# Kernel tuning notes

Measured on AMD Instinct MI355X. Metric: run time of the kernel, lower is better.

Reference implementation:

```python
import jax, jax.numpy as jnp
import numpy as np

B, T, D = 4, 2048, 1024
E, F, K = 8, 4096, 2  # num experts, ffn hidden, top-k


def setup_inputs() -> dict:
    key = jax.random.key(0)
    ks = jax.random.split(key, 7)
    s_in = 1.0 / np.sqrt(D)
    s_ff = 1.0 / np.sqrt(F)
    return {
        "x": jax.random.normal(ks[0], (B, T, D), dtype=jnp.float32),
        "Wg": jax.random.normal(ks[1], (D, E), dtype=jnp.float32) * s_in,
        "bg": jnp.zeros((E,), dtype=jnp.float32),
        "W1": jax.random.normal(ks[2], (E, D, F), dtype=jnp.float32) * s_in,
        "b1": jnp.zeros((E, F), dtype=jnp.float32),
        "W2": jax.random.normal(ks[3], (E, F, D), dtype=jnp.float32) * s_ff,
        "b2": jnp.zeros((E, D), dtype=jnp.float32),
    }


def reference(x, Wg, bg, W1, b1, W2, b2):
    # Gate: per-token expert logits [B, T, E]
    logits = jnp.einsum("btd,de->bte", x, Wg) + bg
    # Top-k per token, softmax over only the selected logits (as in the source)
    topv, topi = jax.lax.top_k(logits, K)          # [B, T, K]
    probs = jax.nn.softmax(topv, axis=-1)           # [B, T, K]
    out = jnp.zeros_like(x)
    # Loop over the small fixed expert set; each expert runs a dense MLP over
    # all tokens, masked/weighted by its routing probability (0 if unselected).
    for e in range(E):
        w = jnp.sum(probs * (topi == e), axis=-1)   # [B, T] combine weight
        h = jax.nn.gelu(jnp.einsum("btd,df->btf", x, W1[e]) + b1[e], approximate=False)
        y = jnp.einsum("btf,fd->btd", h, W2[e]) + b2[e]
        out = out + w[..., None] * y
    return out
```

## Files before the change

### kernel.cpp

```cpp
#include <hip/hip_runtime.h>
#include <cstdint>

#define B_ 4
#define T_ 2048
#define D_ 1024
#define E_ 8
#define F_ 4096
#define K_ 2
#define N_ (B_*T_)
#define NR_ (N_*K_)

#define TM 128
#define BK 64
#define MAXP (NR_ + E_*TM)
#define MAXMB (NR_/TM + E_)
#define MBPX (MAXMB/8)

typedef __attribute__((ext_vector_type(8))) short short8;
typedef __attribute__((ext_vector_type(4))) float f32x4;

typedef const __attribute__((address_space(1))) unsigned int* gp1_t;
typedef __attribute__((address_space(3))) unsigned int* lp3_t;

__device__ __forceinline__ void gl_lds16(const void* g, void* l) {
    __builtin_amdgcn_global_load_lds((gp1_t)g, (lp3_t)l, 16, 0, 0);
}

__device__ __forceinline__ unsigned short f2b(float f) {
    union { float f; unsigned int u; } v; v.f = f;
    unsigned int u = v.u;
    return (unsigned short)((u + 0x7FFFu + ((u >> 16) & 1u)) >> 16);
}

__device__ __forceinline__ float b2f(unsigned short u) {
    union { unsigned int i; float f; } v; v.i = ((unsigned int)u) << 16;
    return v.f;
}

__device__ __forceinline__ float gelu_exact(float x) {
    return 0.5f * x * (1.0f + erff(x * 0.70710678118654752440f));
}

__global__ __launch_bounds__(256) void gate_kernel(
    const float* __restrict__ x, const float* __restrict__ Wg,
    const float* __restrict__ bg, int* __restrict__ topi,
    float* __restrict__ topw, int* __restrict__ counts) {
    int tid  = threadIdx.x;
    int lane = tid & 63;
    int tok  = blockIdx.x * 4 + (tid >> 6);
    int e = lane & 7;
    int c = lane >> 3;
    const float4* xp = (const float4*)(x + (size_t)tok * D_ + c * 128);
    const float*  wp = Wg + (size_t)(c * 128) * E_ + e;
    float acc = 0.f;
    #pragma unroll 8
    for (int i = 0; i < 32; ++i) {
        float4 xv = xp[i];
        acc += xv.x * wp[(i*4+0)*E_];
        acc += xv.y * wp[(i*4+1)*E_];
        acc += xv.z * wp[(i*4+2)*E_];
        acc += xv.w * wp[(i*4+3)*E_];
    }
    acc += __shfl_xor(acc, 8, 64);
    acc += __shfl_xor(acc, 16, 64);
    acc += __shfl_xor(acc, 32, 64);
    float logit = acc + bg[e];
    float v1 = -3.4e38f, v2 = -3.4e38f; int i1 = -1, i2 = -1;
    for (int ee = 0; ee < 8; ++ee) {
        float le = __shfl(logit, ee, 64);
        if (le > v1) { v2 = v1; i2 = i1; v1 = le; i1 = ee; }
        else if (le > v2) { v2 = le; i2 = ee; }
    }
    if (lane == 0) {
        float p2 = expf(v2 - v1);
        float s  = 1.0f + p2;
        topi[tok*2]   = i1; topw[tok*2]   = 1.0f / s;
        topi[tok*2+1] = i2; topw[tok*2+1] = p2 / s;
        atomicAdd(&counts[i1], 1);
        atomicAdd(&counts[i2], 1);
    }
}

__global__ void scan_kernel(const int* __restrict__ counts,
                            int* __restrict__ offs, int* __restrict__ cursors,
                            int* __restrict__ mb_e, int* __restrict__ mb_m0) {
    if (threadIdx.x == 0) {
        int s = 0, mb = 0;
        for (int e = 0; e < E_; ++e) {
            offs[e] = s; cursors[e] = s;
            int nb = (counts[e] + TM - 1) / TM;
            for (int i = 0; i < nb; ++i) { mb_e[mb] = e; mb_m0[mb] = s + i*TM; ++mb; }
            s += nb * TM;
        }
        offs[E_] = s;
        for (int b = mb; b < MAXMB; ++b) mb_e[b] = -1;
    }
}

__global__ __launch_bounds__(256) void scatter_kernel(
    const int* __restrict__ topi, int* __restrict__ cursors,
    int* __restrict__ perm, int* __restrict__ slots) {
    int t = blockIdx.x * blockDim.x + threadIdx.x;
    int lane = threadIdx.x & 63;
    unsigned long long lanebit_m1 = (lane == 63) ? ~0ULL >> 1
                                  : ((1ULL << (lane & 63)) - 1ULL);
    lanebit_m1 = (1ULL << lane) - 1ULL;
    #pragma unroll
    for (int k = 0; k < K_; ++k) {
        int e = (t < N_) ? topi[t*2 + k] : -1;
        int pos = 0;
        #pragma unroll
        for (int ee = 0; ee < E_; ++ee) {
            unsigned long long mask = __ballot(e == ee);
            if (mask) {
                int leader = __ffsll((long long)mask) - 1;
                int base = 0;
                if (lane == leader)
                    base = atomicAdd(&cursors[ee], __popcll(mask));
                base = __shfl(base, leader, 64);
                if (e == ee)
                    pos = base + __popcll(mask & lanebit_m1);
            }
        }
        if (t < N_) {
            perm[pos] = t;
            slots[t*2 + k] = pos;
        }
    }
}

__global__ __launch_bounds__(256) void castx_kernel(
    const float* __restrict__ x, unsigned short* __restrict__ xb) {
    int i = blockIdx.x * blockDim.x + threadIdx.x;
    float4 v = ((const float4*)x)[i];
    ushort4 o; o.x = f2b(v.x); o.y = f2b(v.y); o.z = f2b(v.z); o.w = f2b(v.w);
    ((ushort4*)xb)[i] = o;
}

__global__ __launch_bounds__(256) void tcast_kernel(
    const float* __restrict__ src, unsigned short* __restrict__ dst, int R, int C) {
    __shared__ float tile[64][65];
    int rb = blockIdx.x * 64, cb = blockIdx.y * 64;
    const float* s = src + (size_t)blockIdx.z * R * C;
    unsigned short* d = dst + (size_t)blockIdx.z * R * C;
    int tx = threadIdx.x & 15, ty = threadIdx.x >> 4;
    #pragma unroll
    for (int i = 0; i < 4; ++i) {
        int r = ty + i*16;
        float4 v = *(const float4*)&s[(size_t)(rb + r) * C + cb + tx*4];
        tile[r][tx*4+0] = v.x; tile[r][tx*4+1] = v.y;
        tile[r][tx*4+2] = v.z; tile[r][tx*4+3] = v.w;
    }
    __syncthreads();
    #pragma unroll
    for (int i = 0; i < 4; ++i) {
        int c = ty + i*16;
        ushort4 o;
        o.x = f2b(tile[tx*4+0][c]);
        o.y = f2b(tile[tx*4+1][c]);
        o.z = f2b(tile[tx*4+2][c]);
        o.w = f2b(tile[tx*4+3][c]);
        *(ushort4*)&d[(size_t)(cb + c) * R + rb + tx*4] = o;
    }
}

__global__ __launch_bounds__(256, 4) void ffn1_kernel(
    const unsigned short* __restrict__ Xb, const unsigned short* __restrict__ W1t,
    const float* __restrict__ b1, const int* __restrict__ perm,
    const int* __restrict__ mb_e, const int* __restrict__ mb_m0,
    unsigned short* __restrict__ H) {
    int o   = blockIdx.x + gridDim.x * blockIdx.y;
    int xcd = o & 7;
    int j   = o >> 3;
    int mbi = xcd * MBPX + (j % MBPX);
    int nbi = j / MBPX;
    int e = mb_e[mbi];
    if (e < 0) return;
    int m0 = mb_m0[mbi];
    int n0 = nbi * 128;
    const unsigned short* Bw = W1t + (size_t)e * F_ * D_;

    __shared__ __align__(16) unsigned short lA[128*BK];
    __shared__ __align__(16) unsigned short lB[128*BK];

    int t = threadIdx.x;
    int lane = t & 63;
    int wv = t >> 6;
    int wrow = (wv >> 1) * 64, wcol = (wv & 1) * 64;
    int lr = lane & 15, q = lane >> 4;
    int xork = lr & 7;

    int sr = t >> 3;
    int sc = ((t & 7) ^ (sr & 7)) * 8;
    const unsigned short* pa[4];
    const unsigned short* pb[4];
    #pragma unroll
    for (int i = 0; i < 4; ++i) {
        int tok = perm[m0 + sr + 32*i];
        pa[i] = Xb + (size_t)tok * D_ + sc;
        pb[i] = Bw + (size_t)(n0 + sr + 32*i) * D_ + sc;
    }

    f32x4 acc[4][4];
    #pragma unroll
    for (int mi = 0; mi < 4; ++mi)
        #pragma unroll
        for (int ni = 0; ni < 4; ++ni)
            acc[mi][ni] = (f32x4){0.f, 0.f, 0.f, 0.f};

    for (int kk = 0; kk < D_/BK; ++kk) {
        int k0 = kk * BK;
        #pragma unroll
        for (int i = 0; i < 4; ++i) {
            gl_lds16(pa[i] + k0, &lA[i*2048 + t*8]);
            gl_lds16(pb[i] + k0, &lB[i*2048 + t*8]);
        }
        asm volatile("s_waitcnt vmcnt(0)" ::: "memory");
        __syncthreads();
        #pragma unroll
        for (int s = 0; s < 2; ++s) {
            short8 af[4], bf[4];
            #pragma unroll
            for (int mi = 0; mi < 4; ++mi)
                af[mi] = *(const short8*)&lA[(wrow + mi*16 + lr)*BK + (((s*4+q) ^ xork) * 8)];
            #pragma unroll
            for (int ni = 0; ni < 4; ++ni)
                bf[ni] = *(const short8*)&lB[(wcol + ni*16 + lr)*BK + (((s*4+q) ^ xork) * 8)];
            #pragma unroll
            for (int mi = 0; mi < 4; ++mi)
                #pragma unroll
                for (int ni = 0; ni < 4; ++ni)
                    acc[mi][ni] = __builtin_amdgcn_mfma_f32_16x16x32_bf16(
                        af[mi], bf[ni], acc[mi][ni], 0, 0, 0);
        }
        __syncthreads();
    }

    const float* b1e = b1 + (size_t)e * F_;
    #pragma unroll
    for (int mi = 0; mi < 4; ++mi) {
        int gr = m0 + wrow + mi*16 + q*4;
        #pragma unroll
        for (int ni = 0; ni < 4; ++ni) {
            int f = n0 + wcol + ni*16 + lr;
            float bb = b1e[f];
            #pragma unroll
            for (int r = 0; r < 4; ++r) {
                float h = gelu_exact(acc[mi][ni][r] + bb);
                H[(size_t)(gr + r) * F_ + f] = f2b(h);
            }
        }
    }
}

__global__ __launch_bounds__(256, 4) void ffn2_kernel(
    const unsigned short* __restrict__ H, const unsigned short* __restrict__ W2t,
    const float* __restrict__ b2,
    const int* __restrict__ mb_e, const int* __restrict__ mb_m0,
    unsigned short* __restrict__ Y) {
    int o   = blockIdx.x + gridDim.x * blockIdx.y;
    int xcd = o & 7;
    int j   = o >> 3;
    int mbi = xcd * MBPX + (j % MBPX);
    int nbi = j / MBPX;
    int e = mb_e[mbi];
    if (e < 0) return;
    int m0 = mb_m0[mbi];
    int n0 = nbi * 128;
    const unsigned short* Bw = W2t + (size_t)e * D_ * F_;

    __shared__ __align__(16) unsigned short lA[128*BK];
    __shared__ __align__(16) unsigned short lB[128*BK];

    int t = threadIdx.x;
    int lane = t & 63;
    int wv = t >> 6;
    int wrow = (wv >> 1) * 64, wcol = (wv & 1) * 64;
    int lr = lane & 15, q = lane >> 4;
    int xork = lr & 7;

    int sr = t >> 3;
    int sc = ((t & 7) ^ (sr & 7)) * 8;
    const unsigned short* pa[4];
    const unsigned short* pb[4];
    #pragma unroll
    for (int i = 0; i < 4; ++i) {
        pa[i] = H  + (size_t)(m0 + sr + 32*i) * F_ + sc;
        pb[i] = Bw + (size_t)(n0 + sr + 32*i) * F_ + sc;
    }

    f32x4 acc[4][4];
    #pragma unroll
    for (int mi = 0; mi < 4; ++mi)
        #pragma unroll
        for (int ni = 0; ni < 4; ++ni)
            acc[mi][ni] = (f32x4){0.f, 0.f, 0.f, 0.f};

    for (int kk = 0; kk < F_/BK; ++kk) {
        int k0 = kk * BK;
        #pragma unroll
        for (int i = 0; i < 4; ++i) {
            gl_lds16(pa[i] + k0, &lA[i*2048 + t*8]);
            gl_lds16(pb[i] + k0, &lB[i*2048 + t*8]);
        }
        asm volatile("s_waitcnt vmcnt(0)" ::: "memory");
        __syncthreads();
        #pragma unroll
        for (int s = 0; s < 2; ++s) {
            short8 af[4], bf[4];
            #pragma unroll
            for (int mi = 0; mi < 4; ++mi)
                af[mi] = *(const short8*)&lA[(wrow + mi*16 + lr)*BK + (((s*4+q) ^ xork) * 8)];
            #pragma unroll
            for (int ni = 0; ni < 4; ++ni)
                bf[ni] = *(const short8*)&lB[(wcol + ni*16 + lr)*BK + (((s*4+q) ^ xork) * 8)];
            #pragma unroll
            for (int mi = 0; mi < 4; ++mi)
                #pragma unroll
                for (int ni = 0; ni < 4; ++ni)
                    acc[mi][ni] = __builtin_amdgcn_mfma_f32_16x16x32_bf16(
                        af[mi], bf[ni], acc[mi][ni], 0, 0, 0);
        }
        __syncthreads();
    }

    const float* b2e = b2 + (size_t)e * D_;
    #pragma unroll
    for (int mi = 0; mi < 4; ++mi) {
        int gr = m0 + wrow + mi*16 + q*4;
        #pragma unroll
        for (int ni = 0; ni < 4; ++ni) {
            int dcol = n0 + wcol + ni*16 + lr;
            float bb = b2e[dcol];
            #pragma unroll
            for (int r = 0; r < 4; ++r)
                Y[(size_t)(gr + r) * D_ + dcol] = f2b(acc[mi][ni][r] + bb);
        }
    }
}

__global__ __launch_bounds__(256) void combine_kernel(
    const unsigned short* __restrict__ Y, const int* __restrict__ slots,
    const float* __restrict__ topw, float* __restrict__ out) {
    int t  = blockIdx.x;
    int d4 = threadIdx.x * 4;
    int s0 = slots[t*2], s1 = slots[t*2+1];
    float w0 = topw[t*2], w1 = topw[t*2+1];
    ushort4 y0 = *(const ushort4*)&Y[(size_t)s0 * D_ + d4];
    ushort4 y1 = *(const ushort4*)&Y[(size_t)s1 * D_ + d4];
    float4 o;
    o.x = w0*b2f(y0.x) + w1*b2f(y1.x);
    o.y = w0*b2f(y0.y) + w1*b2f(y1.y);
    o.z = w0*b2f(y0.z) + w1*b2f(y1.z);
    o.w = w0*b2f(y0.w) + w1*b2f(y1.w);
    *(float4*)&out[(size_t)t * D_ + d4] = o;
}

extern "C" void kernel_launch(void* const* d_in, const int* in_sizes, int n_in,
                              void* d_out, int out_size, void* d_ws, size_t ws_size,
                              hipStream_t stream) {
    const float* x  = (const float*)d_in[0];
    const float* Wg = (const float*)d_in[1];
    const float* bg = (const float*)d_in[2];
    const float* W1 = (const float*)d_in[3];
    const float* b1 = (const float*)d_in[4];
    const float* W2 = (const float*)d_in[5];
    const float* b2 = (const float*)d_in[6];
    float* out = (float*)d_out;

    char* wsp = (char*)d_ws;
    size_t off = 0;
    auto alloc = [&](size_t bytes) {
        void* p = wsp + off;
        off += (bytes + 255) & ~(size_t)255;
        return p;
    };
    int*   topi    = (int*)  alloc((size_t)NR_*4);
    float* topw    = (float*)alloc((size_t)NR_*4);
    int*   slots   = (int*)  alloc((size_t)NR_*4);
    int*   counts  = (int*)  alloc(E_*4);
    int*   offs    = (int*)  alloc((E_+1)*4);
    int*   cursors = (int*)  alloc(E_*4);
    int*   mb_e    = (int*)  alloc(MAXMB*4);
    int*   mb_m0   = (int*)  alloc(MAXMB*4);
    int*   perm    = (int*)  alloc((size_t)MAXP*4);
    unsigned short* Xb  = (unsigned short*)alloc((size_t)N_*D_*2);
    unsigned short* W1t = (unsigned short*)alloc((size_t)E_*D_*F_*2);
    unsigned short* W2t = (unsigned short*)alloc((size_t)E_*D_*F_*2);
    unsigned short* Hb  = (unsigned short*)alloc((size_t)MAXP*F_*2);
    unsigned short* Yb  = (unsigned short*)alloc((size_t)MAXP*D_*2);

    hipMemsetAsync(counts, 0, E_*4, stream);
    hipMemsetAsync(perm, 0, (size_t)MAXP*4, stream);

    gate_kernel<<<N_/4, 256, 0, stream>>>(x, Wg, bg, topi, topw, counts);
    scan_kernel<<<1, 64, 0, stream>>>(counts, offs, cursors, mb_e, mb_m0);
    scatter_kernel<<<N_/256, 256, 0, stream>>>(topi, cursors, perm, slots);
    castx_kernel<<<(N_*(size_t)D_/4)/256, 256, 0, stream>>>(x, Xb);
    tcast_kernel<<<dim3(D_/64, F_/64, E_), 256, 0, stream>>>(W1, W1t, D_, F_);
    tcast_kernel<<<dim3(F_/64, D_/64, E_), 256, 0, stream>>>(W2, W2t, F_, D_);
    ffn1_kernel<<<dim3(MAXMB, F_/128), 256, 0, stream>>>(Xb, W1t, b1, perm, mb_e, mb_m0, Hb);
    ffn2_kernel<<<dim3(MAXMB, D_/128), 256, 0, stream>>>(Hb, W2t, b2, mb_e, mb_m0, Yb);
    combine_kernel<<<N_, 256, 0, stream>>>(Yb, slots, topw, out);
}
```

Before: 946.9 us.

## Double-buffer LDS tiles in expert GEMMs and fuse x cast into gate

Both expert FFN GEMM kernels now use two LDS buffers, prefetching the next K tile with global_load_lds while computing the current one. A partial vmcnt wait and raw s_barrier replace the full drain each iteration. Launch bounds drop from 4 to 2 blocks per CU to make room for the doubled shared memory. The separate bf16 cast of x is folded into the gate kernel, which already reads x, saving one launch and one read pass. The cost is lower occupancy and more reliance on correct waitcnt counting.

```diff
diff --git a/kernel.cpp b/kernel.cpp
--- a/kernel.cpp
+++ b/kernel.cpp
@@ -15,6 +15,7 @@
 #define MAXP (NR_ + E_*TM)
 #define MAXMB (NR_/TM + E_)
 #define MBPX (MAXMB/8)
+#define BUFS (128*BK)
 
 typedef __attribute__((ext_vector_type(8))) short short8;
 typedef __attribute__((ext_vector_type(4))) float f32x4;
@@ -44,7 +45,8 @@
 __global__ __launch_bounds__(256) void gate_kernel(
     const float* __restrict__ x, const float* __restrict__ Wg,
     const float* __restrict__ bg, int* __restrict__ topi,
-    float* __restrict__ topw, int* __restrict__ counts) {
+    float* __restrict__ topw, int* __restrict__ counts,
+    unsigned short* __restrict__ Xb) {
     int tid  = threadIdx.x;
     int lane = tid & 63;
     int tok  = blockIdx.x * 4 + (tid >> 6);
@@ -61,6 +63,15 @@
         acc += xv.z * wp[(i*4+2)*E_];
         acc += xv.w * wp[(i*4+3)*E_];
     }
+    {
+        const float4* xw = (const float4*)(x + (size_t)tok * D_ + lane * 16);
+        #pragma unroll
+        for (int j = 0; j < 4; ++j) {
+            float4 v = xw[j];
+            ushort4 o; o.x = f2b(v.x); o.y = f2b(v.y); o.z = f2b(v.z); o.w = f2b(v.w);
+            *(ushort4*)&Xb[(size_t)tok * D_ + lane*16 + j*4] = o;
+        }
+    }
     acc += __shfl_xor(acc, 8, 64);
     acc += __shfl_xor(acc, 16, 64);
     acc += __shfl_xor(acc, 32, 64);
@@ -102,9 +113,7 @@
     int* __restrict__ perm, int* __restrict__ slots) {
     int t = blockIdx.x * blockDim.x + threadIdx.x;
     int lane = threadIdx.x & 63;
-    unsigned long long lanebit_m1 = (lane == 63) ? ~0ULL >> 1
-                                  : ((1ULL << (lane & 63)) - 1ULL);
-    lanebit_m1 = (1ULL << lane) - 1ULL;
+    unsigned long long lanebit_m1 = (1ULL << lane) - 1ULL;
     #pragma unroll
     for (int k = 0; k < K_; ++k) {
         int e = (t < N_) ? topi[t*2 + k] : -1;
@@ -129,14 +138,6 @@
     }
 }
 
-__global__ __launch_bounds__(256) void castx_kernel(
-    const float* __restrict__ x, unsigned short* __restrict__ xb) {
-    int i = blockIdx.x * blockDim.x + threadIdx.x;
-    float4 v = ((const float4*)x)[i];
-    ushort4 o; o.x = f2b(v.x); o.y = f2b(v.y); o.z = f2b(v.z); o.w = f2b(v.w);
-    ((ushort4*)xb)[i] = o;
-}
-
 __global__ __launch_bounds__(256) void tcast_kernel(
     const float* __restrict__ src, unsigned short* __restrict__ dst, int R, int C) {
     __shared__ float tile[64][65];
@@ -164,7 +165,7 @@
     }
 }
 
-__global__ __launch_bounds__(256, 4) void ffn1_kernel(
+__global__ __launch_bounds__(256, 2) void ffn1_kernel(
     const unsigned short* __restrict__ Xb, const unsigned short* __restrict__ W1t,
     const float* __restrict__ b1, const int* __restrict__ perm,
     const int* __restrict__ mb_e, const int* __restrict__ mb_m0,
@@ -180,8 +181,8 @@
     int n0 = nbi * 128;
     const unsigned short* Bw = W1t + (size_t)e * F_ * D_;
 
-    __shared__ __align__(16) unsigned short lA[128*BK];
-    __shared__ __align__(16) unsigned short lB[128*BK];
+    __shared__ __align__(16) unsigned short lA[2*BUFS];
+    __shared__ __align__(16) unsigned short lB[2*BUFS];
 
     int t = threadIdx.x;
     int lane = t & 63;
@@ -208,24 +209,38 @@
         for (int ni = 0; ni < 4; ++ni)
             acc[mi][ni] = (f32x4){0.f, 0.f, 0.f, 0.f};
 
-    for (int kk = 0; kk < D_/BK; ++kk) {
-        int k0 = kk * BK;
-        #pragma unroll
-        for (int i = 0; i < 4; ++i) {
-            gl_lds16(pa[i] + k0, &lA[i*2048 + t*8]);
-            gl_lds16(pb[i] + k0, &lB[i*2048 + t*8]);
-        }
-        asm volatile("s_waitcnt vmcnt(0)" ::: "memory");
-        __syncthreads();
+    #pragma unroll
+    for (int i = 0; i < 4; ++i) {
+        gl_lds16(pa[i], &lA[i*2048 + t*8]);
+        gl_lds16(pb[i], &lB[i*2048 + t*8]);
+    }
+
+    const int KT = D_/BK;
+    for (int kk = 0; kk < KT; ++kk) {
+        int cur = (kk & 1) * BUFS;
+        if (kk + 1 < KT) {
+            int nxt = ((kk+1) & 1) * BUFS;
+            int k0 = (kk+1) * BK;
+            #pragma unroll
+            for (int i = 0; i < 4; ++i) {
+                gl_lds16(pa[i] + k0, &lA[nxt + i*2048 + t*8]);
+                gl_lds16(pb[i] + k0, &lB[nxt + i*2048 + t*8]);
+            }
+            asm volatile("s_waitcnt vmcnt(8)" ::: "memory");
+        } else {
+            asm volatile("s_waitcnt vmcnt(0)" ::: "memory");
+        }
+        __builtin_amdgcn_s_barrier();
+        __builtin_amdgcn_sched_barrier(0);
         #pragma unroll
         for (int s = 0; s < 2; ++s) {
             short8 af[4], bf[4];
             #pragma unroll
             for (int mi = 0; mi < 4; ++mi)
-                af[mi] = *(const short8*)&lA[(wrow + mi*16 + lr)*BK + (((s*4+q) ^ xork) * 8)];
+                af[mi] = *(const short8*)&lA[cur + (wrow + mi*16 + lr)*BK + (((s*4+q) ^ xork) * 8)];
             #pragma unroll
             for (int ni = 0; ni < 4; ++ni)
-                bf[ni] = *(const short8*)&lB[(wcol + ni*16 + lr)*BK + (((s*4+q) ^ xork) * 8)];
+                bf[ni] = *(const short8*)&lB[cur + (wcol + ni*16 + lr)*BK + (((s*4+q) ^ xork) * 8)];
             #pragma unroll
             for (int mi = 0; mi < 4; ++mi)
                 #pragma unroll
@@ -233,7 +248,8 @@
                     acc[mi][ni] = __builtin_amdgcn_mfma_f32_16x16x32_bf16(
                         af[mi], bf[ni], acc[mi][ni], 0, 0, 0);
         }
-        __syncthreads();
+        __builtin_amdgcn_sched_barrier(0);
+        __builtin_amdgcn_s_barrier();
     }
 
     const float* b1e = b1 + (size_t)e * F_;
@@ -253,7 +269,7 @@
     }
 }
 
-__global__ __launch_bounds__(256, 4) void ffn2_kernel(
+__global__ __launch_bounds__(256, 2) void ffn2_kernel(
     const unsigned short* __restrict__ H, const unsigned short* __restrict__ W2t,
     const float* __restrict__ b2,
     const int* __restrict__ mb_e, const int* __restrict__ mb_m0,
@@ -269,8 +285,8 @@
     int n0 = nbi * 128;
     const unsigned short* Bw = W2t + (size_t)e * D_ * F_;
 
-    __shared__ __align__(16) unsigned short lA[128*BK];
-    __shared__ __align__(16) unsigned short lB[128*BK];
+    __shared__ __align__(16) unsigned short lA[2*BUFS];
+    __shared__ __align__(16) unsigned short lB[2*BUFS];
 
     int t = threadIdx.x;
     int lane = t & 63;
@@ -296,24 +312,38 @@
         for (int ni = 0; ni < 4; ++ni)
             acc[mi][ni] = (f32x4){0.f, 0.f, 0.f, 0.f};
 
-    for (int kk = 0; kk < F_/BK; ++kk) {
-        int k0 = kk * BK;
-        #pragma unroll
-        for (int i = 0; i < 4; ++i) {
-            gl_lds16(pa[i] + k0, &lA[i*2048 + t*8]);
-            gl_lds16(pb[i] + k0, &lB[i*2048 + t*8]);
-        }
-        asm volatile("s_waitcnt vmcnt(0)" ::: "memory");
-        __syncthreads();
+    #pragma unroll
+    for (int i = 0; i < 4; ++i) {
+        gl_lds16(pa[i], &lA[i*2048 + t*8]);
+        gl_lds16(pb[i], &lB[i*2048 + t*8]);
+    }
+
+    const int KT = F_/BK;
+    for (int kk = 0; kk < KT; ++kk) {
+        int cur = (kk & 1) * BUFS;
+        if (kk + 1 < KT) {
+            int nxt = ((kk+1) & 1) * BUFS;
+            int k0 = (kk+1) * BK;
+            #pragma unroll
+            for (int i = 0; i < 4; ++i) {
+                gl_lds16(pa[i] + k0, &lA[nxt + i*2048 + t*8]);
+                gl_lds16(pb[i] + k0, &lB[nxt + i*2048 + t*8]);
+            }
+            asm volatile("s_waitcnt vmcnt(8)" ::: "memory");
+        } else {
+            asm volatile("s_waitcnt vmcnt(0)" ::: "memory");
+        }
+        __builtin_amdgcn_s_barrier();
+        __builtin_amdgcn_sched_barrier(0);
         #pragma unroll
         for (int s = 0; s < 2; ++s) {
             short8 af[4], bf[4];
             #pragma unroll
             for (int mi = 0; mi < 4; ++mi)
-                af[mi] = *(const short8*)&lA[(wrow + mi*16 + lr)*BK + (((s*4+q) ^ xork) * 8)];
+                af[mi] = *(const short8*)&lA[cur + (wrow + mi*16 + lr)*BK + (((s*4+q) ^ xork) * 8)];
             #pragma unroll
             for (int ni = 0; ni < 4; ++ni)
-                bf[ni] = *(const short8*)&lB[(wcol + ni*16 + lr)*BK + (((s*4+q) ^ xork) * 8)];
+                bf[ni] = *(const short8*)&lB[cur + (wcol + ni*16 + lr)*BK + (((s*4+q) ^ xork) * 8)];
             #pragma unroll
             for (int mi = 0; mi < 4; ++mi)
                 #pragma unroll
@@ -321,7 +351,8 @@
                     acc[mi][ni] = __builtin_amdgcn_mfma_f32_16x16x32_bf16(
                         af[mi], bf[ni], acc[mi][ni], 0, 0, 0);
         }
-        __syncthreads();
+        __builtin_amdgcn_sched_barrier(0);
+        __builtin_amdgcn_s_barrier();
     }
 
     const float* b2e = b2 + (size_t)e * D_;
@@ -393,10 +424,9 @@
     hipMemsetAsync(counts, 0, E_*4, stream);
     hipMemsetAsync(perm, 0, (size_t)MAXP*4, stream);
 
-    gate_kernel<<<N_/4, 256, 0, stream>>>(x, Wg, bg, topi, topw, counts);
+    gate_kernel<<<N_/4, 256, 0, stream>>>(x, Wg, bg, topi, topw, counts, Xb);
     scan_kernel<<<1, 64, 0, stream>>>(counts, offs, cursors, mb_e, mb_m0);
     scatter_kernel<<<N_/256, 256, 0, stream>>>(topi, cursors, perm, slots);
-    castx_kernel<<<(N_*(size_t)D_/4)/256, 256, 0, stream>>>(x, Xb);
     tcast_kernel<<<dim3(D_/64, F_/64, E_), 256, 0, stream>>>(W1, W1t, D_, F_);
     tcast_kernel<<<dim3(F_/64, D_/64, E_), 256, 0, stream>>>(W2, W2t, F_, D_);
     ffn1_kernel<<<dim3(MAXMB, F_/128), 256, 0, stream>>>(Xb, W1t, b1, perm, mb_e, mb_m0, Hb);
```

Measured after the change: 1.101 ms. 16.3% more time.

## Rewrite FFN1 as a 256x256 double-buffered ping-pong MFMA GEMM, fuse x cast

Applied to the files above, without the earlier changes.

The first expert GEMM moves to 256x256 tiles computed by 512 threads (8 waves). LDS is double-buffered, and the global-to-LDS loads for upcoming K tiles are interleaved with MFMA quarters under explicit barriers, priority bumps and vmcnt waits. Expert row blocks are padded to 256 for FFN1 and 128 for FFN2, each with its own block list. The bf16 cast of x is folded into the gate kernel, which removes one launch and one extra read of x. The goal is higher MFMA utilisation and less load stall in the dominant GEMM, at the cost of more padding waste, lower occupancy and fragile hand-written synchronisation.

```diff
diff --git a/kernel.cpp b/kernel.cpp
--- a/kernel.cpp
+++ b/kernel.cpp
@@ -10,11 +10,14 @@
 #define N_ (B_*T_)
 #define NR_ (N_*K_)
 
-#define TM 128
+#define TM1 256
+#define TM2 128
 #define BK 64
-#define MAXP (NR_ + E_*TM)
-#define MAXMB (NR_/TM + E_)
-#define MBPX (MAXMB/8)
+#define MAXP (NR_ + E_*TM1)
+#define MB1 (NR_/TM1 + E_)
+#define MB2 (NR_/TM2 + E_)
+#define MBPX1 (MB1/8)
+#define MBPX2 (MB2/8)
 
 typedef __attribute__((ext_vector_type(8))) short short8;
 typedef __attribute__((ext_vector_type(4))) float f32x4;
@@ -44,7 +47,8 @@
 __global__ __launch_bounds__(256) void gate_kernel(
     const float* __restrict__ x, const float* __restrict__ Wg,
     const float* __restrict__ bg, int* __restrict__ topi,
-    float* __restrict__ topw, int* __restrict__ counts) {
+    float* __restrict__ topw, int* __restrict__ counts,
+    unsigned short* __restrict__ Xb) {
     int tid  = threadIdx.x;
     int lane = tid & 63;
     int tok  = blockIdx.x * 4 + (tid >> 6);
@@ -61,6 +65,15 @@
         acc += xv.z * wp[(i*4+2)*E_];
         acc += xv.w * wp[(i*4+3)*E_];
     }
+    {
+        const float4* xw = (const float4*)(x + (size_t)tok * D_ + lane * 16);
+        #pragma unroll
+        for (int j = 0; j < 4; ++j) {
+            float4 v = xw[j];
+            ushort4 o; o.x = f2b(v.x); o.y = f2b(v.y); o.z = f2b(v.z); o.w = f2b(v.w);
+            *(ushort4*)&Xb[(size_t)tok * D_ + lane*16 + j*4] = o;
+        }
+    }
     acc += __shfl_xor(acc, 8, 64);
     acc += __shfl_xor(acc, 16, 64);
     acc += __shfl_xor(acc, 32, 64);
@@ -83,17 +96,22 @@
 
 __global__ void scan_kernel(const int* __restrict__ counts,
                             int* __restrict__ offs, int* __restrict__ cursors,
-                            int* __restrict__ mb_e, int* __restrict__ mb_m0) {
+                            int* __restrict__ mb1_e, int* __restrict__ mb1_m0,
+                            int* __restrict__ mb2_e, int* __restrict__ mb2_m0) {
     if (threadIdx.x == 0) {
-        int s = 0, mb = 0;
+        int s = 0, a = 0, b = 0;
         for (int e = 0; e < E_; ++e) {
             offs[e] = s; cursors[e] = s;
-            int nb = (counts[e] + TM - 1) / TM;
-            for (int i = 0; i < nb; ++i) { mb_e[mb] = e; mb_m0[mb] = s + i*TM; ++mb; }
-            s += nb * TM;
+            int c = counts[e];
+            int nb1 = (c + TM1 - 1) / TM1;
+            for (int i = 0; i < nb1; ++i) { mb1_e[a] = e; mb1_m0[a] = s + i*TM1; ++a; }
+            int nb2 = (c + TM2 - 1) / TM2;
+            for (int i = 0; i < nb2; ++i) { mb2_e[b] = e; mb2_m0[b] = s + i*TM2; ++b; }
+            s += nb1 * TM1;
         }
         offs[E_] = s;
-        for (int b = mb; b < MAXMB; ++b) mb_e[b] = -1;
+        for (; a < MB1; ++a) mb1_e[a] = -1;
+        for (; b < MB2; ++b) mb2_e[b] = -1;
     }
 }
 
@@ -102,9 +120,7 @@
     int* __restrict__ perm, int* __restrict__ slots) {
     int t = blockIdx.x * blockDim.x + threadIdx.x;
     int lane = threadIdx.x & 63;
-    unsigned long long lanebit_m1 = (lane == 63) ? ~0ULL >> 1
-                                  : ((1ULL << (lane & 63)) - 1ULL);
-    lanebit_m1 = (1ULL << lane) - 1ULL;
+    unsigned long long lanebit_m1 = (1ULL << lane) - 1ULL;
     #pragma unroll
     for (int k = 0; k < K_; ++k) {
         int e = (t < N_) ? topi[t*2 + k] : -1;
@@ -129,14 +145,6 @@
     }
 }
 
-__global__ __launch_bounds__(256) void castx_kernel(
-    const float* __restrict__ x, unsigned short* __restrict__ xb) {
-    int i = blockIdx.x * blockDim.x + threadIdx.x;
-    float4 v = ((const float4*)x)[i];
-    ushort4 o; o.x = f2b(v.x); o.y = f2b(v.y); o.z = f2b(v.z); o.w = f2b(v.w);
-    ((ushort4*)xb)[i] = o;
-}
-
 __global__ __launch_bounds__(256) void tcast_kernel(
     const float* __restrict__ src, unsigned short* __restrict__ dst, int R, int C) {
     __shared__ float tile[64][65];
@@ -164,90 +172,162 @@
     }
 }
 
-__global__ __launch_bounds__(256, 4) void ffn1_kernel(
+__global__ __launch_bounds__(512, 2) void ffn1_kernel(
     const unsigned short* __restrict__ Xb, const unsigned short* __restrict__ W1t,
     const float* __restrict__ b1, const int* __restrict__ perm,
-    const int* __restrict__ mb_e, const int* __restrict__ mb_m0,
+    const int* __restrict__ mb1_e, const int* __restrict__ mb1_m0,
     unsigned short* __restrict__ H) {
     int o   = blockIdx.x + gridDim.x * blockIdx.y;
     int xcd = o & 7;
-    int j   = o >> 3;
-    int mbi = xcd * MBPX + (j % MBPX);
-    int nbi = j / MBPX;
-    int e = mb_e[mbi];
+    int jj  = o >> 3;
+    int mbi = xcd * MBPX1 + jj % MBPX1;
+    int nbi = jj / MBPX1;
+    int e = mb1_e[mbi];
     if (e < 0) return;
-    int m0 = mb_m0[mbi];
-    int n0 = nbi * 128;
+    int m0 = mb1_m0[mbi];
+    int n0 = nbi * 256;
     const unsigned short* Bw = W1t + (size_t)e * F_ * D_;
 
-    __shared__ __align__(16) unsigned short lA[128*BK];
-    __shared__ __align__(16) unsigned short lB[128*BK];
-
-    int t = threadIdx.x;
-    int lane = t & 63;
-    int wv = t >> 6;
-    int wrow = (wv >> 1) * 64, wcol = (wv & 1) * 64;
-    int lr = lane & 15, q = lane >> 4;
-    int xork = lr & 7;
-
-    int sr = t >> 3;
-    int sc = ((t & 7) ^ (sr & 7)) * 8;
-    const unsigned short* pa[4];
-    const unsigned short* pb[4];
-    #pragma unroll
-    for (int i = 0; i < 4; ++i) {
-        int tok = perm[m0 + sr + 32*i];
-        pa[i] = Xb + (size_t)tok * D_ + sc;
-        pb[i] = Bw + (size_t)(n0 + sr + 32*i) * D_ + sc;
-    }
-
-    f32x4 acc[4][4];
-    #pragma unroll
-    for (int mi = 0; mi < 4; ++mi)
-        #pragma unroll
-        for (int ni = 0; ni < 4; ++ni)
-            acc[mi][ni] = (f32x4){0.f, 0.f, 0.f, 0.f};
-
-    for (int kk = 0; kk < D_/BK; ++kk) {
-        int k0 = kk * BK;
-        #pragma unroll
-        for (int i = 0; i < 4; ++i) {
-            gl_lds16(pa[i] + k0, &lA[i*2048 + t*8]);
-            gl_lds16(pb[i] + k0, &lB[i*2048 + t*8]);
-        }
-        asm volatile("s_waitcnt vmcnt(0)" ::: "memory");
-        __syncthreads();
-        #pragma unroll
-        for (int s = 0; s < 2; ++s) {
-            short8 af[4], bf[4];
-            #pragma unroll
-            for (int mi = 0; mi < 4; ++mi)
-                af[mi] = *(const short8*)&lA[(wrow + mi*16 + lr)*BK + (((s*4+q) ^ xork) * 8)];
-            #pragma unroll
-            for (int ni = 0; ni < 4; ++ni)
-                bf[ni] = *(const short8*)&lB[(wcol + ni*16 + lr)*BK + (((s*4+q) ^ xork) * 8)];
-            #pragma unroll
-            for (int mi = 0; mi < 4; ++mi)
+    __shared__ __align__(16) unsigned short lA[32768];
+    __shared__ __align__(16) unsigned short lB[32768];
+
+    int t = threadIdx.x, lane = t & 63, wid = t >> 6;
+    int wm = wid >> 2, wn = wid & 3;
+    int lr = lane & 15, q = lane >> 4, xork = lr & 7;
+    int bh = wn >> 1, bro = (wn & 1) * 64;
+
+    int srow = t >> 3;
+    int swch = ((t & 7) ^ (srow & 7)) * 8;
+    const unsigned short* pA[2][2];
+    const unsigned short* pB[2][2];
+    #pragma unroll
+    for (int h = 0; h < 2; ++h)
+        #pragma unroll
+        for (int l = 0; l < 2; ++l) {
+            int r = srow + l * 64;
+            pA[h][l] = Xb + (size_t)perm[m0 + h*128 + r] * D_ + swch;
+            pB[h][l] = Bw + (size_t)(n0 + h*128 + r) * D_ + swch;
+        }
+
+    f32x4 acc[8][4];
+    #pragma unroll
+    for (int m = 0; m < 8; ++m)
+        #pragma unroll
+        for (int n = 0; n < 4; ++n)
+            acc[m][n] = (f32x4){0.f, 0.f, 0.f, 0.f};
+
+#define STG_B(tile, h) do { int _s = ((tile)&1)*16384 + (h)*8192; int _k = (tile)*BK; \
+        gl_lds16(pB[h][0] + _k, &lB[_s + t*8]); \
+        gl_lds16(pB[h][1] + _k, &lB[_s + 4096 + t*8]); } while (0)
+#define STG_A(tile, h) do { int _s = ((tile)&1)*16384 + (h)*8192; int _k = (tile)*BK; \
+        gl_lds16(pA[h][0] + _k, &lA[_s + t*8]); \
+        gl_lds16(pA[h][1] + _k, &lA[_s + 4096 + t*8]); } while (0)
+
+    STG_B(0, 0); STG_B(0, 1); STG_A(0, 0); STG_A(0, 1);
+    asm volatile("s_waitcnt vmcnt(4)" ::: "memory");
+    STG_B(1, 0); STG_B(1, 1); STG_A(1, 0);
+    asm volatile("s_waitcnt vmcnt(6)" ::: "memory");
+    __builtin_amdgcn_s_barrier();
+
+    const int KT = D_ / BK;
+    for (int tt = 0; tt < KT; ++tt) {
+        int cur = (tt & 1) * 16384;
+        short8 af[8][2], bf[4][2];
+        #pragma unroll
+        for (int m = 0; m < 4; ++m)
+            #pragma unroll
+            for (int s = 0; s < 2; ++s)
+                af[m][s] = *(const short8*)&lA[cur + wm*8192 + (m*16+lr)*64 + (((s*4+q)^xork)*8)];
+        #pragma unroll
+        for (int n = 0; n < 4; ++n)
+            #pragma unroll
+            for (int s = 0; s < 2; ++s)
+                bf[n][s] = *(const short8*)&lB[cur + bh*8192 + (bro + n*16 + lr)*64 + (((s*4+q)^xork)*8)];
+        if (tt + 1 < KT) STG_A(tt + 1, 1);
+        __builtin_amdgcn_sched_barrier(0);
+        __builtin_amdgcn_s_barrier();
+        asm volatile("s_waitcnt lgkmcnt(0)" ::: "memory");
+        __builtin_amdgcn_sched_barrier(0);
+        __builtin_amdgcn_s_setprio(1);
+        #pragma unroll
+        for (int m = 0; m < 4; ++m)
+            #pragma unroll
+            for (int n = 0; n < 2; ++n)
                 #pragma unroll
-                for (int ni = 0; ni < 4; ++ni)
-                    acc[mi][ni] = __builtin_amdgcn_mfma_f32_16x16x32_bf16(
-                        af[mi], bf[ni], acc[mi][ni], 0, 0, 0);
-        }
-        __syncthreads();
-    }
+                for (int s = 0; s < 2; ++s)
+                    acc[m][n] = __builtin_amdgcn_mfma_f32_16x16x32_bf16(af[m][s], bf[n][s], acc[m][n], 0, 0, 0);
+        __builtin_amdgcn_s_setprio(0);
+        __builtin_amdgcn_sched_barrier(0);
+        __builtin_amdgcn_s_barrier();
+        #pragma unroll
+        for (int m = 4; m < 8; ++m)
+            #pragma unroll
+            for (int s = 0; s < 2; ++s)
+                af[m][s] = *(const short8*)&lA[cur + wm*8192 + (m*16+lr)*64 + (((s*4+q)^xork)*8)];
+        if (tt + 2 < KT) STG_B(tt + 2, 0);
+        __builtin_amdgcn_sched_barrier(0);
+        __builtin_amdgcn_s_barrier();
+        asm volatile("s_waitcnt lgkmcnt(0)" ::: "memory");
+        __builtin_amdgcn_sched_barrier(0);
+        __builtin_amdgcn_s_setprio(1);
+        #pragma unroll
+        for (int m = 0; m < 4; ++m)
+            #pragma unroll
+            for (int n = 2; n < 4; ++n)
+                #pragma unroll
+                for (int s = 0; s < 2; ++s)
+                    acc[m][n] = __builtin_amdgcn_mfma_f32_16x16x32_bf16(af[m][s], bf[n][s], acc[m][n], 0, 0, 0);
+        __builtin_amdgcn_s_setprio(0);
+        __builtin_amdgcn_sched_barrier(0);
+        __builtin_amdgcn_s_barrier();
+        if (tt + 2 < KT) STG_B(tt + 2, 1);
+        __builtin_amdgcn_sched_barrier(0);
+        __builtin_amdgcn_s_barrier();
+        __builtin_amdgcn_sched_barrier(0);
+        __builtin_amdgcn_s_setprio(1);
+        #pragma unroll
+        for (int m = 4; m < 8; ++m)
+            #pragma unroll
+            for (int n = 0; n < 2; ++n)
+                #pragma unroll
+                for (int s = 0; s < 2; ++s)
+                    acc[m][n] = __builtin_amdgcn_mfma_f32_16x16x32_bf16(af[m][s], bf[n][s], acc[m][n], 0, 0, 0);
+        __builtin_amdgcn_s_setprio(0);
+        __builtin_amdgcn_sched_barrier(0);
+        __builtin_amdgcn_s_barrier();
+        if (tt + 2 < KT) STG_A(tt + 2, 0);
+        __builtin_amdgcn_sched_barrier(0);
+        __builtin_amdgcn_s_barrier();
+        __builtin_amdgcn_sched_barrier(0);
+        __builtin_amdgcn_s_setprio(1);
+        #pragma unroll
+        for (int m = 4; m < 8; ++m)
+            #pragma unroll
+            for (int n = 2; n < 4; ++n)
+                #pragma unroll
+                for (int s = 0; s < 2; ++s)
+                    acc[m][n] = __builtin_amdgcn_mfma_f32_16x16x32_bf16(af[m][s], bf[n][s], acc[m][n], 0, 0, 0);
+        __builtin_amdgcn_s_setprio(0);
+        __builtin_amdgcn_sched_barrier(0);
+        if (tt < KT - 2) { asm volatile("s_waitcnt vmcnt(6)" ::: "memory"); }
+        else             { asm volatile("s_waitcnt vmcnt(0)" ::: "memory"); }
+        __builtin_amdgcn_s_barrier();
+    }
+#undef STG_A
+#undef STG_B
 
     const float* b1e = b1 + (size_t)e * F_;
     #pragma unroll
-    for (int mi = 0; mi < 4; ++mi) {
-        int gr = m0 + wrow + mi*16 + q*4;
-        #pragma unroll
-        for (int ni = 0; ni < 4; ++ni) {
-            int f = n0 + wcol + ni*16 + lr;
-            float bb = b1e[f];
+    for (int m = 0; m < 8; ++m) {
+        int gr = m0 + wm*128 + m*16 + q*4;
+        #pragma unroll
+        for (int n = 0; n < 4; ++n) {
+            int fc = n0 + wn*64 + n*16 + lr;
+            float bb = b1e[fc];
             #pragma unroll
             for (int r = 0; r < 4; ++r) {
-                float h = gelu_exact(acc[mi][ni][r] + bb);
-                H[(size_t)(gr + r) * F_ + f] = f2b(h);
+                float h = gelu_exact(acc[m][n][r] + bb);
+                H[(size_t)(gr + r) * F_ + fc] = f2b(h);
             }
         }
     }
@@ -256,16 +336,16 @@
 __global__ __launch_bounds__(256, 4) void ffn2_kernel(
     const unsigned short* __restrict__ H, const unsigned short* __restrict__ W2t,
     const float* __restrict__ b2,
-    const int* __restrict__ mb_e, const int* __restrict__ mb_m0,
+    const int* __restrict__ mb2_e, const int* __restrict__ mb2_m0,
     unsigned short* __restrict__ Y) {
     int o   = blockIdx.x + gridDim.x * blockIdx.y;
     int xcd = o & 7;
     int j   = o >> 3;
-    int mbi = xcd * MBPX + (j % MBPX);
-    int nbi = j / MBPX;
-    int e = mb_e[mbi];
+    int mbi = xcd * MBPX2 + (j % MBPX2);
+    int nbi = j / MBPX2;
+    int e = mb2_e[mbi];
     if (e < 0) return;
-    int m0 = mb_m0[mbi];
+    int m0 = mb2_m0[mbi];
     int n0 = nbi * 128;
     const unsigned short* Bw = W2t + (size_t)e * D_ * F_;
 
@@ -381,8 +461,10 @@
     int*   counts  = (int*)  alloc(E_*4);
     int*   offs    = (int*)  alloc((E_+1)*4);
     int*   cursors = (int*)  alloc(E_*4);
-    int*   mb_e    = (int*)  alloc(MAXMB*4);
-    int*   mb_m0   = (int*)  alloc(MAXMB*4);
+    int*   mb1_e   = (int*)  alloc(MB1*4);
+    int*   mb1_m0  = (int*)  alloc(MB1*4);
+    int*   mb2_e   = (int*)  alloc(MB2*4);
+    int*   mb2_m0  = (int*)  alloc(MB2*4);
     int*   perm    = (int*)  alloc((size_t)MAXP*4);
     unsigned short* Xb  = (unsigned short*)alloc((size_t)N_*D_*2);
     unsigned short* W1t = (unsigned short*)alloc((size_t)E_*D_*F_*2);
@@ -393,13 +475,12 @@
     hipMemsetAsync(counts, 0, E_*4, stream);
     hipMemsetAsync(perm, 0, (size_t)MAXP*4, stream);
 
-    gate_kernel<<<N_/4, 256, 0, stream>>>(x, Wg, bg, topi, topw, counts);
-    scan_kernel<<<1, 64, 0, stream>>>(counts, offs, cursors, mb_e, mb_m0);
+    gate_kernel<<<N_/4, 256, 0, stream>>>(x, Wg, bg, topi, topw, counts, Xb);
+    scan_kernel<<<1, 64, 0, stream>>>(counts, offs, cursors, mb1_e, mb1_m0, mb2_e, mb2_m0);
     scatter_kernel<<<N_/256, 256, 0, stream>>>(topi, cursors, perm, slots);
-    castx_kernel<<<(N_*(size_t)D_/4)/256, 256, 0, stream>>>(x, Xb);
     tcast_kernel<<<dim3(D_/64, F_/64, E_), 256, 0, stream>>>(W1, W1t, D_, F_);
     tcast_kernel<<<dim3(F_/64, D_/64, E_), 256, 0, stream>>>(W2, W2t, F_, D_);
-    ffn1_kernel<<<dim3(MAXMB, F_/128), 256, 0, stream>>>(Xb, W1t, b1, perm, mb_e, mb_m0, Hb);
-    ffn2_kernel<<<dim3(MAXMB, D_/128), 256, 0, stream>>>(Hb, W2t, b2, mb_e, mb_m0, Yb);
+    ffn1_kernel<<<dim3(MB1, F_/256), 512, 0, stream>>>(Xb, W1t, b1, perm, mb1_e, mb1_m0, Hb);
+    ffn2_kernel<<<dim3(MB2, D_/128), 256, 0, stream>>>(Hb, W2t, b2, mb2_e, mb2_m0, Yb);
     combine_kernel<<<N_, 256, 0, stream>>>(Yb, slots, topw, out);
 }
```

Result: slower. 1.043 ms (+10.2%).
